# Kernel tuning notes

Hardware: AMD Instinct MI355X
Metric: run time of the kernel (lower is better)

The kernel has to match this reference:

```python
import math
import jax, jax.numpy as jnp
import numpy as np
from jax import lax

SAMPLE_RATE = 16000
BLOCK_SIZE = 64
B = 524288


def setup_inputs() -> dict:
    key = jax.random.key(0)
    k1, k2, k3 = jax.random.split(key, 3)
    fm_params = jax.random.uniform(k1, (B, 1, 6), dtype=jnp.float32)
    # realistic fundamentals in [50, 400) Hz; module clamps to >=1 anyway
    f0_hz = 50.0 + 350.0 * jax.random.uniform(k2, (B, 1), dtype=jnp.float32)
    phase_state = jax.random.uniform(k3, (B, 4), dtype=jnp.float32)
    return {"fm_params": fm_params, "f0_hz": f0_hz, "phase_state": phase_state}


def reference(fm_params, f0_hz, phase_state):
    # T == 1 (module requirement), so squeeze the frame dim everywhere.
    dtype = fm_params.dtype
    two_pi = 2.0 * math.pi

    f0 = jnp.clip(f0_hz[:, 0], 1.0, None)            # [B]
    p = fm_params[:, 0, :]                            # [B, 6]
    # parameter mappings (op1 mod depth p[:,0] is unused, as in the original)
    r1 = 0.25 + p[:, 1] * 15.75
    fb1 = p[:, 2] * 0.95
    d2 = p[:, 3] * 10.0
    r2 = 0.25 + p[:, 4] * 15.75
    fb2 = p[:, 5] * 0.95

    inc1 = two_pi * f0 * r1 / SAMPLE_RATE             # [B]
    inc2 = two_pi * f0 * r2 / SAMPLE_RATE

    start1 = phase_state[:, 0]                        # frame start phases
    start2 = phase_state[:, 1]
    last1_0 = phase_state[:, 2]                       # feedback buffers
    last2_0 = phase_state[:, 3]

    offsets = jnp.arange(BLOCK_SIZE, dtype=dtype)     # [S]
    # per-sample phases, scanned over the sample axis: [S, B]
    phase1 = start1[None, :] + offsets[:, None] * inc1[None, :]
    phase2 = start2[None, :] + offsets[:, None] * inc2[None, :]

    def step(carry, ph):
        l1, l2 = carry
        ph1, ph2 = ph
        o1 = jnp.sin(ph1 + fb1 * l1)                  # op1 with self-feedback
        o2 = jnp.sin(ph2 + d2 * o1 + fb2 * l2)        # op2 carrier, FM'd by op1
        return (o1, o2), o2

    (l1f, l2f), samples = lax.scan(step, (last1_0, last2_0), (phase1, phase2))
    audio = samples.T                                 # [B, S]

    rms = jnp.sqrt(jnp.mean(audio * audio, axis=-1, keepdims=True) + 1e-5)
    audio = audio / rms

    phase_end = jnp.stack(
        [
            (start1 + BLOCK_SIZE * inc1) % two_pi,
            (start2 + BLOCK_SIZE * inc2) % two_pi,
            l1f,
            l2f,
        ],
        axis=-1,
    )                                                 # [B, 4]
    return audio, phase_end
```

## Files before the change

kernel.cpp:

```cpp
#include <hip/hip_runtime.h>

#define NBLOCK 64

__device__ __forceinline__ float fast_sinf(float x) {
    float kf = rintf(x * 0.63661977236758134f);
    int   q  = (int)kf;
    float r = fmaf(kf, -1.5707963705062866f, x);
    r = fmaf(kf, 4.3711390001862171e-8f, r);
    float z = r * r;
    float s = fmaf(z, fmaf(z, -1.9515295891e-4f, 8.3321608736e-3f), -1.6666654611e-1f);
    float sinr = fmaf(z * r, s, r);
    float c = fmaf(z, fmaf(z, 2.4433157118e-5f, -1.3887316255e-3f), 4.1666645683e-2f);
    float cosr = fmaf(z, fmaf(z, c, -0.5f), 1.0f);
    float res = (q & 1) ? cosr : sinr;
    return (q & 2) ? -res : res;
}

__device__ __forceinline__ float mod_two_pi(float x) {
    const float Y = 6.2831853071795864769f;
    float kf = floorf(__fdiv_rn(x, Y));
    float m = fmaf(-kf, Y, x);
    if (m < 0.0f)  { kf -= 1.0f; m = fmaf(-kf, Y, x); }
    if (m >= Y)    { kf += 1.0f; m = fmaf(-kf, Y, x); }
    return m;
}

__global__ __launch_bounds__(256)
void fm_synth_kernel(const float* __restrict__ fm_params,
                     const float* __restrict__ f0_hz,
                     const float* __restrict__ phase_state,
                     float* __restrict__ out, int nv)
{
    __shared__ float lds[NBLOCK * 256];

    int tid = threadIdx.x;
    int b   = blockIdx.x * 256 + tid;
    int bc  = min(b, nv - 1);
    bool live = (b < nv);

    const float2* fm2 = (const float2*)fm_params;
    float2 p01 = fm2[bc * 3 + 0];
    float2 p23 = fm2[bc * 3 + 1];
    float2 p45 = fm2[bc * 3 + 2];
    float  f0  = fmaxf(f0_hz[bc], 1.0f);
    float4 st  = ((const float4*)phase_state)[bc];

    const float TWO_PI = 6.2831853071795864769f;
    float r1  = __fadd_rn(0.25f, __fmul_rn(p01.y, 15.75f));
    float fb1 = __fmul_rn(p23.x, 0.95f);
    float d2  = __fmul_rn(p23.y, 10.0f);
    float r2  = __fadd_rn(0.25f, __fmul_rn(p45.x, 15.75f));
    float fb2 = __fmul_rn(p45.y, 0.95f);
    float inc1 = __fdiv_rn(__fmul_rn(__fmul_rn(TWO_PI, f0), r1), 16000.0f);
    float inc2 = __fdiv_rn(__fmul_rn(__fmul_rn(TWO_PI, f0), r2), 16000.0f);

    float start1 = st.x, start2 = st.y;
    float l1 = st.z, l2 = st.w;

    float ss = 0.0f;
    int sw = tid;
#pragma unroll
    for (int t = 0; t < NBLOCK; ++t) {
        if ((t & 3) == 0) sw = (tid + t) & 255;
        float tf  = (float)t;
        float ph1 = tf * inc1 + start1;
        float ph2 = tf * inc2 + start2;
        float o1 = fast_sinf(ph1 + fb1 * l1);
        float o2 = fast_sinf(ph2 + d2 * o1 + fb2 * l2);
        l1 = o1;
        l2 = o2;
        lds[t * 256 + sw] = o2;
        ss = fmaf(o2, o2, ss);
    }
    float inv = 1.0f / sqrtf(ss * 0.015625f + 1e-5f);

    __syncthreads();

    int lane = tid & 63;
    int w    = tid >> 6;
    int q    = lane >> 4;
    int t4   = lane & 15;
    float4* out4 = (float4*)out;
    int blockBase = blockIdx.x * 256;
#pragma unroll
    for (int k = 0; k < 16; ++k) {
        int vv = 4 * k + q;
        float invk = __shfl(inv, vv, 64);
        int v = w * 64 + vv;
        int sw2 = (v + 4 * t4) & 255;
        const float* src = &lds[(4 * t4) * 256 + sw2];
        float4 val;
        val.x = src[0]     * invk;
        val.y = src[256]   * invk;
        val.z = src[512]   * invk;
        val.w = src[768]   * invk;
        if (blockBase + v < nv)
            out4[(size_t)(blockBase + v) * 16 + t4] = val;
    }

    float x1 = __fadd_rn(start1, __fmul_rn(64.0f, inc1));
    float x2 = __fadd_rn(start2, __fmul_rn(64.0f, inc2));
    float4 pe;
    pe.x = mod_two_pi(x1);
    pe.y = mod_two_pi(x2);
    pe.z = l1;
    pe.w = l2;
    if (live)
        ((float4*)(out + (size_t)nv * NBLOCK))[b] = pe;
}

extern "C" void kernel_launch(void* const* d_in, const int* in_sizes, int n_in,
                              void* d_out, int out_size, void* d_ws, size_t ws_size,
                              hipStream_t stream) {
    const float* fm_params   = (const float*)d_in[0];
    const float* f0_hz       = (const float*)d_in[1];
    const float* phase_state = (const float*)d_in[2];
    float* out = (float*)d_out;
    int nv = in_sizes[1];
    int grid = (nv + 255) / 256;
    fm_synth_kernel<<<grid, 256, 0, stream>>>(fm_params, f0_hz, phase_state, out, nv);
}
```

Before: 177.1 us.

## Shrink blocks to one wavefront and partially unroll the synthesis loop

Blocks shrink from 256 to 64 threads, each with a 16 KB LDS tile instead of 64 KB. This lets more blocks share a CU, and the barrier only spans one wavefront. The 64-step sample loop becomes an outer non-unrolled loop over groups of four, and the store loop is unrolled by 4. Both reduce code size and register pressure. The cost is four times as many blocks and per-iteration loop overhead in the serial recurrence.

```diff
diff --git a/kernel.cpp b/kernel.cpp
--- a/kernel.cpp
+++ b/kernel.cpp
@@ -25,17 +25,17 @@
     return m;
 }
 
-__global__ __launch_bounds__(256)
+__global__ __launch_bounds__(64)
 void fm_synth_kernel(const float* __restrict__ fm_params,
                      const float* __restrict__ f0_hz,
                      const float* __restrict__ phase_state,
                      float* __restrict__ out, int nv)
 {
-    __shared__ float lds[NBLOCK * 256];
+    __shared__ float lds[NBLOCK * 64];
 
-    int tid = threadIdx.x;
-    int b   = blockIdx.x * 256 + tid;
-    int bc  = min(b, nv - 1);
+    int lane = threadIdx.x;
+    int b    = blockIdx.x * 64 + lane;
+    int bc   = min(b, nv - 1);
     bool live = (b < nv);
 
     const float2* fm2 = (const float2*)fm_params;
@@ -58,44 +58,45 @@
     float l1 = st.z, l2 = st.w;
 
     float ss = 0.0f;
-    int sw = tid;
+#pragma unroll 1
+    for (int j = 0; j < 16; ++j) {
+        int sw = (lane + 4 * j) & 63;
+        float* row = &lds[4 * j * 64 + sw];
+        float tj = (float)(4 * j);
 #pragma unroll
-    for (int t = 0; t < NBLOCK; ++t) {
-        if ((t & 3) == 0) sw = (tid + t) & 255;
-        float tf  = (float)t;
-        float ph1 = tf * inc1 + start1;
-        float ph2 = tf * inc2 + start2;
-        float o1 = fast_sinf(ph1 + fb1 * l1);
-        float o2 = fast_sinf(ph2 + d2 * o1 + fb2 * l2);
-        l1 = o1;
-        l2 = o2;
-        lds[t * 256 + sw] = o2;
-        ss = fmaf(o2, o2, ss);
+        for (int c = 0; c < 4; ++c) {
+            float tf  = tj + (float)c;
+            float ph1 = fmaf(tf, inc1, start1);
+            float ph2 = fmaf(tf, inc2, start2);
+            float o1 = fast_sinf(fmaf(fb1, l1, ph1));
+            float o2 = fast_sinf(fmaf(fb2, l2, fmaf(d2, o1, ph2)));
+            l1 = o1;
+            l2 = o2;
+            row[c * 64] = o2;
+            ss = fmaf(o2, o2, ss);
+        }
     }
     float inv = 1.0f / sqrtf(ss * 0.015625f + 1e-5f);
 
     __syncthreads();
 
-    int lane = tid & 63;
-    int w    = tid >> 6;
-    int q    = lane >> 4;
-    int t4   = lane & 15;
+    int q  = lane >> 4;
+    int t4 = lane & 15;
     float4* out4 = (float4*)out;
-    int blockBase = blockIdx.x * 256;
-#pragma unroll
+    int blockBase = blockIdx.x * 64;
+    const float* srcRow = &lds[4 * t4 * 64];
+#pragma unroll 4
     for (int k = 0; k < 16; ++k) {
         int vv = 4 * k + q;
         float invk = __shfl(inv, vv, 64);
-        int v = w * 64 + vv;
-        int sw2 = (v + 4 * t4) & 255;
-        const float* src = &lds[(4 * t4) * 256 + sw2];
+        const float* s = srcRow + ((vv + 4 * t4) & 63);
         float4 val;
-        val.x = src[0]     * invk;
-        val.y = src[256]   * invk;
-        val.z = src[512]   * invk;
-        val.w = src[768]   * invk;
-        if (blockBase + v < nv)
-            out4[(size_t)(blockBase + v) * 16 + t4] = val;
+        val.x = s[0]   * invk;
+        val.y = s[64]  * invk;
+        val.z = s[128] * invk;
+        val.w = s[192] * invk;
+        if (blockBase + vv < nv)
+            out4[(size_t)(blockBase + vv) * 16 + t4] = val;
     }
 
     float x1 = __fadd_rn(start1, __fmul_rn(64.0f, inc1));
@@ -117,6 +118,6 @@
     const float* phase_state = (const float*)d_in[2];
     float* out = (float*)d_out;
     int nv = in_sizes[1];
-    int grid = (nv + 255) / 256;
-    fm_synth_kernel<<<grid, 256, 0, stream>>>(fm_params, f0_hz, phase_state, out, nv);
+    int grid = (nv + 63) / 64;
+    fm_synth_kernel<<<grid, 64, 0, stream>>>(fm_params, f0_hz, phase_state, out, nv);
 }
```

New measurement: 176.6 us. Within noise of the previous version (-0.3%).
